# Optimization experiments

Measured on AMD Instinct MI355X. Metric: run time of the kernel, lower is better.

## Reference

```python
import jax, jax.numpy as jnp
import numpy as np

B, L, P, K, D, H = 8192, 224, 6, 5, 128, 4
S = K * K                 # 25 spatial positions in the patch
CENTER = S // 2           # central target pixel index
SCALE_RANGE = 0.2
BN_EPS = 1e-5


def _uniform(k, shape, fan_in):
    s = 1.0 / np.sqrt(fan_in)
    return jax.random.uniform(k, shape, jnp.float32, -s, s)


def setup_inputs() -> dict:
    key = jax.random.key(0)
    ks = jax.random.split(key, 32)
    inp = {}
    inp["x"] = jax.random.normal(ks[0], (B, L, K, K), jnp.float32)
    # attention projections (stored as (in, out), applied as x @ W + b)
    inp["wk_w"] = _uniform(ks[1], (L, D), L); inp["wk_b"] = _uniform(ks[2], (D,), L)
    inp["wv_w"] = _uniform(ks[3], (L, D), L); inp["wv_b"] = _uniform(ks[4], (D,), L)
    inp["wq_w"] = _uniform(ks[5], (L, D), L); inp["wq_b"] = _uniform(ks[6], (D,), L)
    inp["ng_w"] = _uniform(ks[7], (D, 1), D); inp["ng_b"] = _uniform(ks[8], (1,), D)
    # ffn branch: GLU(128->64) -> BN -> GLU(64->P)
    inp["f1_fw"] = _uniform(ks[9], (D, 64), D);  inp["f1_fb"] = _uniform(ks[10], (64,), D)
    inp["f1_gw"] = _uniform(ks[11], (D, 64), D); inp["f1_gb"] = _uniform(ks[12], (64,), D)
    inp["f_bn_g"] = jnp.ones((64,), jnp.float32); inp["f_bn_b"] = jnp.zeros((64,), jnp.float32)
    inp["f2_fw"] = _uniform(ks[13], (64, P), 64); inp["f2_fb"] = _uniform(ks[14], (P,), 64)
    inp["f2_gw"] = _uniform(ks[15], (64, P), 64); inp["f2_gb"] = _uniform(ks[16], (P,), 64)
    # scalar branch: same shapes
    inp["s1_fw"] = _uniform(ks[17], (D, 64), D);  inp["s1_fb"] = _uniform(ks[18], (64,), D)
    inp["s1_gw"] = _uniform(ks[19], (D, 64), D);  inp["s1_gb"] = _uniform(ks[20], (64,), D)
    inp["s_bn_g"] = jnp.ones((64,), jnp.float32); inp["s_bn_b"] = jnp.zeros((64,), jnp.float32)
    inp["s2_fw"] = _uniform(ks[21], (64, P), 64); inp["s2_fb"] = _uniform(ks[22], (P,), 64)
    inp["s2_gw"] = _uniform(ks[23], (64, P), 64); inp["s2_gb"] = _uniform(ks[24], (P,), 64)
    # endmember spectra (P, L), nonnegative as typical for HSI
    inp["endmember"] = jax.random.uniform(ks[25], (P, L), jnp.float32)
    return inp


def _swish(x):
    return x * jax.nn.sigmoid(x)


def _glu(x, fw, fb, gw, gb):
    return (x @ fw + fb) * jax.nn.sigmoid(x @ gw + gb)


def _bn_train(x, g, b):
    # BatchNorm1d training-mode forward: biased batch stats over batch dim
    m = jnp.mean(x, axis=0)
    v = jnp.var(x, axis=0)
    return (x - m) * jax.lax.rsqrt(v + BN_EPS) * g + b


def _forward(x, wk_w, wk_b, wv_w, wv_b, wq_w, wq_b, ng_w, ng_b,
             f1_fw, f1_fb, f1_gw, f1_gb, f_bn_g, f_bn_b, f2_fw, f2_fb, f2_gw, f2_gb,
             s1_fw, s1_fb, s1_gw, s1_gb, s_bn_g, s_bn_b, s2_fw, s2_fb, s2_gw, s2_gb,
             endmember):
    b = x.shape[0]
    xt = x.reshape(b, L, S).transpose(0, 2, 1)        # (B, S, L)
    keys = xt @ wk_w + wk_b                            # (B, S, D)
    vals = xt @ wv_w + wv_b                            # (B, S, D)
    q = xt[:, CENTER] @ wq_w + wq_b                    # (B, D)
    dk, dv = D // H, D // H
    kh = keys.reshape(b, S, H, dk)
    qh = q.reshape(b, H, dk)
    # note: scaling uses full key_dim (np.sqrt(self.key_dim)), not per-head dim
    scores = jnp.einsum('bhd,bshd->bhs', qh, kh) / np.sqrt(D).astype(np.float32)
    mask = jnp.zeros((S,), jnp.float32).at[CENTER].set(-1e6)
    att = jax.nn.softmax(scores + mask, axis=-1)       # (B, H, S)
    vh = vals.reshape(b, S, H, dv)
    surround = jnp.einsum('bhs,bshd->bhd', att, vh).reshape(b, D)
    central = vals[:, CENTER]                          # (B, D)
    nearby = jax.nn.sigmoid((central - surround) @ ng_w + ng_b)  # (B, 1)
    ss = central + nearby * surround                   # (B, D) spatial-spectral feature

    h = _glu(_swish(ss), f1_fw, f1_fb, f1_gw, f1_gb)
    h = _swish(_bn_train(h, f_bn_g, f_bn_b))
    abd = jax.nn.softmax(_glu(h, f2_fw, f2_fb, f2_gw, f2_gb), axis=1)  # (B, P)

    g = _glu(_swish(ss), s1_fw, s1_fb, s1_gw, s1_gb)
    g = _swish(_bn_train(g, s_bn_g, s_bn_b))
    edm_scale = jnp.tanh(_glu(g, s2_fw, s2_fb, s2_gw, s2_gb))          # (B, P)

    scale = 1.0 + SCALE_RANGE * edm_scale[:, :, None]  # (B, P, 1)
    edm = scale * endmember[None]                      # (B, P, L)
    recon = jnp.einsum('bp,bpl->bl', abd, edm)         # (B, L)
    return recon, abd, edm_scale


def reference(x, wk_w, wk_b, wv_w, wv_b, wq_w, wq_b, ng_w, ng_b,
              f1_fw, f1_fb, f1_gw, f1_gb, f_bn_g, f_bn_b, f2_fw, f2_fb, f2_gw, f2_gb,
              s1_fw, s1_fb, s1_gw, s1_gb, s_bn_g, s_bn_b, s2_fw, s2_fb, s2_gw, s2_gb,
              endmember):
    return _forward(x, wk_w, wk_b, wv_w, wv_b, wq_w, wq_b, ng_w, ng_b,
                    f1_fw, f1_fb, f1_gw, f1_gb, f_bn_g, f_bn_b, f2_fw, f2_fb, f2_gw, f2_gb,
                    s1_fw, s1_fb, s1_gw, s1_gb, s_bn_g, s_bn_b, s2_fw, s2_fb, s2_gw, s2_gb,
                    endmember)
```

## Files before the change

### kernel.cpp

```cpp
#include <hip/hip_runtime.h>
#include <hip/hip_bf16.h>

typedef unsigned short ushort;
typedef unsigned int   uint;
typedef __bf16 bfrag_t __attribute__((ext_vector_type(8)));
typedef float  ffrag_t __attribute__((ext_vector_type(4)));

#define NB   8192
#define LL   224
#define SS   25
#define CTR  12
#define DD   128
#define PP   6
#define HID  64
#define GPB  2
#define NKC  7
#define NMT  4
#define NNT  24
#define VST  132
#define WPK_ELEMS (NKC * NNT * 64 * 8)
#define FC1_ELEMS (4 * 16 * 64 * 8)

__device__ __forceinline__ float f_sigmoid(float x) { return 1.0f / (1.0f + __expf(-x)); }
__device__ __forceinline__ ushort f2bf(float f) {
    __hip_bfloat16 h = __float2bfloat16(f);
    ushort u; __builtin_memcpy(&u, &h, 2); return u;
}
__device__ __forceinline__ float bfu2f(ushort u) {
    uint v = ((uint)u) << 16; float f; __builtin_memcpy(&f, &v, 4); return f;
}

__global__ __launch_bounds__(256) void k0_pack(
    const float* __restrict__ wk_w, const float* __restrict__ wv_w,
    const float* __restrict__ wq_w,
    const float* __restrict__ f1_fw, const float* __restrict__ f1_gw,
    const float* __restrict__ s1_fw, const float* __restrict__ s1_gw,
    ushort* __restrict__ wpack, ushort* __restrict__ fc1pack,
    float* __restrict__ stats)
{
    const int blk = blockIdx.x;
    if (blk == 0) stats[threadIdx.x] = 0.f;
    if (blk < NNT) {
        const int nt  = blk;
        const int mat = nt >> 3;
        const float* w = mat == 0 ? wk_w : (mat == 1 ? wv_w : wq_w);
        const int cb = (nt & 7) * 16;
        for (int e = threadIdx.x; e < NKC * 64 * 8; e += 256) {
            int j    = e & 7;
            int lane = (e >> 3) & 63;
            int kc   = e >> 9;
            int k = kc * 32 + ((lane >> 4) << 3) + j;
            int c = cb + (lane & 15);
            wpack[((kc * NNT + nt) * 64 + lane) * 8 + j] = f2bf(w[k * DD + c]);
        }
    } else {
        const int nt = blk - NNT;
        const int m2 = nt >> 2;
        const float* w = m2 == 0 ? f1_fw : (m2 == 1 ? f1_gw : (m2 == 2 ? s1_fw : s1_gw));
        const int cb = (nt & 3) * 16;
        for (int e = threadIdx.x; e < 4 * 64 * 8; e += 256) {
            int j    = e & 7;
            int lane = (e >> 3) & 63;
            int kc   = e >> 9;
            int k = kc * 32 + ((lane >> 4) << 3) + j;
            int c = cb + (lane & 15);
            fc1pack[((kc * 16 + nt) * 64 + lane) * 8 + j] = f2bf(w[k * HID + c]);
        }
    }
}

__global__ __launch_bounds__(512, 4) void kA_front(
    const float* __restrict__ x,
    const ushort* __restrict__ wpack,
    const float* __restrict__ wk_b, const float* __restrict__ wv_b,
    const float* __restrict__ wq_b,
    const float* __restrict__ ng_w, const float* __restrict__ ng_b,
    ushort* __restrict__ swv_ws)
{
    __shared__ ushort alds[NMT * NKC * 64 * 8];
    __shared__ float  qv[GPB * DD];
    __shared__ float  att[8 * 26];
    __shared__ float  red[4];

    const int t    = threadIdx.x;
    const int b0   = blockIdx.x * GPB;
    const int wave = t >> 6;
    const int lane = t & 63;

    const int cC = wave * 16 + (lane & 15);
    const float biask = wk_b[cC];
    const float biasv = wv_b[cC];
    const float biasq = wq_b[cC];
    const float ngw   = ng_w[t & 127];

    const float4* xb4 = (const float4*)(x + (size_t)b0 * (LL * SS));
    float4 xf[6];
#pragma unroll
    for (int k = 0; k < 6; ++k) {
        int q = t + k * 512;
        if (q < 2800) xf[k] = xb4[q];
    }
#pragma unroll
    for (int k = 0; k < 6; ++k) {
        int q = t + k * 512;
        if (q < 2800) {
            int e0 = q * 4;
            int g  = e0 >= 5600;
            int eb0 = e0 - g * 5600;
#pragma unroll
            for (int c = 0; c < 4; ++c) {
                int eb = eb0 + c;
                int l = eb / 25;
                int s = eb - l * 25;
                int r = g * 32 + s;
                int idx = (((r >> 4) * NKC + (l >> 5)) * 64 +
                           ((r & 15) | (((l >> 3) & 3) << 4))) * 8 + (l & 7);
                float fv = c == 0 ? xf[k].x : c == 1 ? xf[k].y : c == 2 ? xf[k].z : xf[k].w;
                alds[idx] = f2bf(fv);
            }
        }
    }
    __syncthreads();

    ffrag_t acck[NMT], accv[NMT], accq[2];
#pragma unroll
    for (int mt = 0; mt < NMT; ++mt) {
        acck[mt] = ffrag_t{0.f, 0.f, 0.f, 0.f};
        accv[mt] = ffrag_t{0.f, 0.f, 0.f, 0.f};
    }
    accq[0] = ffrag_t{0.f, 0.f, 0.f, 0.f};
    accq[1] = ffrag_t{0.f, 0.f, 0.f, 0.f};

    bfrag_t bk = *(const bfrag_t*)(wpack + ((0 * NNT + wave) * 64 + lane) * 8);
    bfrag_t bv = *(const bfrag_t*)(wpack + ((0 * NNT + wave + 8) * 64 + lane) * 8);
    bfrag_t bq = *(const bfrag_t*)(wpack + ((0 * NNT + wave + 16) * 64 + lane) * 8);
#pragma unroll
    for (int kc = 0; kc < NKC; ++kc) {
        bfrag_t nbk, nbv, nbq;
        if (kc + 1 < NKC) {
            nbk = *(const bfrag_t*)(wpack + (((kc + 1) * NNT + wave) * 64 + lane) * 8);
            nbv = *(const bfrag_t*)(wpack + (((kc + 1) * NNT + wave + 8) * 64 + lane) * 8);
            nbq = *(const bfrag_t*)(wpack + (((kc + 1) * NNT + wave + 16) * 64 + lane) * 8);
        }
#pragma unroll
        for (int mt = 0; mt < NMT; ++mt) {
            bfrag_t af = *(const bfrag_t*)(alds + ((mt * NKC + kc) * 64 + lane) * 8);
            acck[mt] = __builtin_amdgcn_mfma_f32_16x16x32_bf16(af, bk, acck[mt], 0, 0, 0);
            accv[mt] = __builtin_amdgcn_mfma_f32_16x16x32_bf16(af, bv, accv[mt], 0, 0, 0);
            if ((mt & 1) == 0)
                accq[mt >> 1] = __builtin_amdgcn_mfma_f32_16x16x32_bf16(af, bq, accq[mt >> 1], 0, 0, 0);
        }
        if (kc + 1 < NKC) { bk = nbk; bv = nbv; bq = nbq; }
    }
    __syncthreads();

    {
#pragma unroll
        for (int mt = 0; mt < NMT; ++mt) {
#pragma unroll
            for (int reg = 0; reg < 4; ++reg) {
                int r = mt * 16 + ((lane >> 4) << 2) + reg;
                int g = r >> 5;
                int s = r & 31;
                if (s < SS) {
                    alds[(g * SS + s) * VST + cC]        = f2bf(acck[mt][reg] + biask);
                    alds[6600 + (g * SS + s) * VST + cC] = f2bf(accv[mt][reg] + biasv);
                }
            }
        }
        if ((lane >> 4) == 3) {
            qv[cC]      = accq[0][0] + biasq;
            qv[DD + cC] = accq[1][0] + biasq;
        }
    }
    __syncthreads();

    if (t < 256) {
        const int r   = t >> 5;
        const int g   = r >> 2;
        const int h   = r & 3;
        const int l32 = t & 31;
        float sc = -1e30f;
        if (l32 < SS) {
            const ushort* kr = alds + (g * SS + l32) * VST + h * 32;
            const float*  qr = qv + g * DD + h * 32;
            float a0 = 0.f, a1 = 0.f, a2 = 0.f, a3 = 0.f;
#pragma unroll
            for (int i = 0; i < 32; i += 4) {
                a0 = fmaf(qr[i + 0], bfu2f(kr[i + 0]), a0);
                a1 = fmaf(qr[i + 1], bfu2f(kr[i + 1]), a1);
                a2 = fmaf(qr[i + 2], bfu2f(kr[i + 2]), a2);
                a3 = fmaf(qr[i + 3], bfu2f(kr[i + 3]), a3);
            }
            sc = ((a0 + a1) + (a2 + a3)) * 0.088388347648318447f;
            if (l32 == CTR) sc -= 1e6f;
        }
        float mx = sc;
#pragma unroll
        for (int m = 16; m > 0; m >>= 1) mx = fmaxf(mx, __shfl_xor(mx, m, 32));
        float e = __expf(sc - mx);
        float sum = e;
#pragma unroll
        for (int m = 16; m > 0; m >>= 1) sum += __shfl_xor(sum, m, 32);
        if (l32 < SS) att[r * 26 + l32] = e / sum;
    }
    __syncthreads();

    if (t < 256) {
        const int g = t >> 7;
        const int d = t & 127;
        const int h = d >> 5;
        const ushort* vrow = alds + 6600 + g * SS * VST + d;
        const float* arow = att + (g * 4 + h) * 26;
        float s0 = 0.f, s1 = 0.f;
#pragma unroll
        for (int s = 0; s < 24; s += 2) {
            s0 = fmaf(arow[s],     bfu2f(vrow[s * VST]),       s0);
            s1 = fmaf(arow[s + 1], bfu2f(vrow[(s + 1) * VST]), s1);
        }
        float sur = fmaf(arow[24], bfu2f(vrow[24 * VST]), s0 + s1);
        float cen = bfu2f(vrow[CTR * VST]);
        float term = (cen - sur) * ngw;
#pragma unroll
        for (int off = 32; off > 0; off >>= 1) term += __shfl_down(term, off);
        if (lane == 0) red[wave] = term;
        __syncthreads();
        float tot = red[g * 2] + red[g * 2 + 1] + ng_b[0];
        float nearby = f_sigmoid(tot);
        float ssv = cen + nearby * sur;
        float sw  = ssv * f_sigmoid(ssv);
        swv_ws[(size_t)(b0 + g) * DD + d] = f2bf(sw);
    } else {
        __syncthreads();
    }
}

__global__ __launch_bounds__(256) void kC_fc1(
    const ushort* __restrict__ swv_ws,
    const ushort* __restrict__ fc1pack,
    const float* __restrict__ f1_fb, const float* __restrict__ f1_gb,
    const float* __restrict__ s1_fb, const float* __restrict__ s1_gb,
    float* __restrict__ h1_ws, float* __restrict__ g1_ws,
    float* __restrict__ stats)
{
    const int t    = threadIdx.x;
    const int wave = t >> 6;
    const int lane = t & 63;
    const int m0   = blockIdx.x * 32;
    const int c16  = wave * 16 + (lane & 15);

    const float fb1 = f1_fb[c16], gb1 = f1_gb[c16];
    const float fb2 = s1_fb[c16], gb2 = s1_gb[c16];

    ffrag_t acc[4][2];
#pragma unroll
    for (int ni = 0; ni < 4; ++ni)
#pragma unroll
        for (int mt = 0; mt < 2; ++mt) acc[ni][mt] = ffrag_t{0.f, 0.f, 0.f, 0.f};

#pragma unroll
    for (int kc = 0; kc < 4; ++kc) {
        bfrag_t bf[4];
#pragma unroll
        for (int ni = 0; ni < 4; ++ni) {
            int nt = wave + 4 * ni;
            bf[ni] = *(const bfrag_t*)(fc1pack + ((kc * 16 + nt) * 64 + lane) * 8);
        }
#pragma unroll
        for (int mt = 0; mt < 2; ++mt) {
            bfrag_t af = *(const bfrag_t*)(swv_ws +
                (size_t)(m0 + mt * 16 + (lane & 15)) * DD + kc * 32 + ((lane >> 4) << 3));
#pragma unroll
            for (int ni = 0; ni < 4; ++ni)
                acc[ni][mt] = __builtin_amdgcn_mfma_f32_16x16x32_bf16(af, bf[ni], acc[ni][mt], 0, 0, 0);
        }
    }

    float hs = 0.f, hq = 0.f, gs = 0.f, gq = 0.f;
#pragma unroll
    for (int mt = 0; mt < 2; ++mt) {
#pragma unroll
        for (int reg = 0; reg < 4; ++reg) {
            int m = m0 + mt * 16 + ((lane >> 4) << 2) + reg;
            float hv = (acc[0][mt][reg] + fb1) * f_sigmoid(acc[1][mt][reg] + gb1);
            float gv = (acc[2][mt][reg] + fb2) * f_sigmoid(acc[3][mt][reg] + gb2);
            h1_ws[(size_t)m * HID + c16] = hv;
            g1_ws[(size_t)m * HID + c16] = gv;
            hs += hv; hq = fmaf(hv, hv, hq);
            gs += gv; gq = fmaf(gv, gv, gq);
        }
    }
    hs += __shfl_xor(hs, 16); hs += __shfl_xor(hs, 32);
    hq += __shfl_xor(hq, 16); hq += __shfl_xor(hq, 32);
    gs += __shfl_xor(gs, 16); gs += __shfl_xor(gs, 32);
    gq += __shfl_xor(gq, 16); gq += __shfl_xor(gq, 32);
    const int cg = lane >> 4;
    float val = cg == 0 ? hs : cg == 1 ? hq : cg == 2 ? gs : gq;
    atomicAdd(&stats[cg * 64 + c16], val);
}

#define K3G 32
__global__ __launch_bounds__(256) void k3_back(
    const float* __restrict__ h1, const float* __restrict__ g1,
    const float* __restrict__ stats,
    const float* __restrict__ f_bng, const float* __restrict__ f_bnb,
    const float* __restrict__ s_bng, const float* __restrict__ s_bnb,
    const float* __restrict__ f2_fw, const float* __restrict__ f2_fb,
    const float* __restrict__ f2_gw, const float* __restrict__ f2_gb,
    const float* __restrict__ s2_fw, const float* __restrict__ s2_fb,
    const float* __restrict__ s2_gw, const float* __restrict__ s2_gb,
    const float* __restrict__ endm,
    float* __restrict__ out_recon, float* __restrict__ out_abd,
    float* __restrict__ out_es)
{
    const int B0 = blockIdx.x * K3G;
    const int t = threadIdx.x;
    __shared__ float bnl[256];
    __shared__ float w2[4][HID * PP];
    __shared__ float b2[4][8];
    __shared__ float endl[PP * LL];
    __shared__ float hh[K3G * 65], gg[K3G * 65];
    __shared__ float logit[K3G * 8], esv[K3G * 8], coef[K3G * 8];

    if (t < 128) {
        int br = t >> 6, j = t & 63;
        float S1 = stats[br * 128 + j];
        float S2 = stats[br * 128 + 64 + j];
        float m   = S1 * (1.0f / NB);
        float var = S2 * (1.0f / NB) - m * m;
        float gam = br ? s_bng[j] : f_bng[j];
        float be  = br ? s_bnb[j] : f_bnb[j];
        float a   = gam * rsqrtf(var + 1e-5f);
        bnl[br * 128 + j]      = a;
        bnl[br * 128 + 64 + j] = be - m * a;
    }
    for (int i = t; i < HID * PP; i += 256) {
        w2[0][i] = f2_fw[i];
        w2[1][i] = f2_gw[i];
        w2[2][i] = s2_fw[i];
        w2[3][i] = s2_gw[i];
    }
    if (t < PP) {
        b2[0][t] = f2_fb[t];
        b2[1][t] = f2_gb[t];
        b2[2][t] = s2_fb[t];
        b2[3][t] = s2_gb[t];
    }
    for (int i = t; i < PP * LL; i += 256) endl[i] = endm[i];
    __syncthreads();

    for (int i = t; i < K3G * HID; i += 256) {
        int ba = i >> 6, j = i & 63;
        float v1 = h1[(size_t)(B0 + ba) * HID + j] * bnl[j] + bnl[64 + j];
        hh[ba * 65 + j] = v1 * f_sigmoid(v1);
        float v2 = g1[(size_t)(B0 + ba) * HID + j] * bnl[128 + j] + bnl[192 + j];
        gg[ba * 65 + j] = v2 * f_sigmoid(v2);
    }
    __syncthreads();

    for (int i = t; i < K3G * 2 * PP; i += 256) {
        int ba = i / (2 * PP);
        int rr = i - ba * (2 * PP);
        int br = rr / PP;
        int p  = rr - br * PP;
        const float* src = (br ? gg : hh) + ba * 65;
        const float* fw  = w2[br * 2];
        const float* gw  = w2[br * 2 + 1];
        float df = b2[br * 2][p], dg = b2[br * 2 + 1][p];
#pragma unroll 8
        for (int j = 0; j < HID; ++j) {
            float v = src[j];
            df = fmaf(v, fw[j * PP + p], df);
            dg = fmaf(v, gw[j * PP + p], dg);
        }
        float glu = df * f_sigmoid(dg);
        if (br == 0) {
            logit[ba * 8 + p] = glu;
        } else {
            float e = tanhf(glu);
            esv[ba * 8 + p] = e;
            out_es[(size_t)(B0 + ba) * PP + p] = e;
        }
    }
    __syncthreads();

    if (t < K3G) {
        float mx = -1e30f;
#pragma unroll
        for (int p = 0; p < PP; ++p) mx = fmaxf(mx, logit[t * 8 + p]);
        float e[PP]; float sum = 0.f;
#pragma unroll
        for (int p = 0; p < PP; ++p) { e[p] = __expf(logit[t * 8 + p] - mx); sum += e[p]; }
        float inv = 1.0f / sum;
#pragma unroll
        for (int p = 0; p < PP; ++p) {
            float a = e[p] * inv;
            out_abd[(size_t)(B0 + t) * PP + p] = a;
            coef[t * 8 + p] = a * (1.0f + 0.2f * esv[t * 8 + p]);
        }
    }
    __syncthreads();

    for (int i = t; i < K3G * LL; i += 256) {
        int ba = i / LL;
        int l  = i - ba * LL;
        float r = 0.f;
#pragma unroll
        for (int p = 0; p < PP; ++p)
            r = fmaf(coef[ba * 8 + p], endl[p * LL + l], r);
        out_recon[(size_t)(B0 + ba) * LL + l] = r;
    }
}

extern "C" void kernel_launch(void* const* d_in, const int* in_sizes, int n_in,
                              void* d_out, int out_size, void* d_ws, size_t ws_size,
                              hipStream_t stream)
{
    const float* x     = (const float*)d_in[0];
    const float* wk_w  = (const float*)d_in[1];
    const float* wk_b  = (const float*)d_in[2];
    const float* wv_w  = (const float*)d_in[3];
    const float* wv_b  = (const float*)d_in[4];
    const float* wq_w  = (const float*)d_in[5];
    const float* wq_b  = (const float*)d_in[6];
    const float* ng_w  = (const float*)d_in[7];
    const float* ng_b  = (const float*)d_in[8];
    const float* f1_fw = (const float*)d_in[9];
    const float* f1_fb = (const float*)d_in[10];
    const float* f1_gw = (const float*)d_in[11];
    const float* f1_gb = (const float*)d_in[12];
    const float* f_bng = (const float*)d_in[13];
    const float* f_bnb = (const float*)d_in[14];
    const float* f2_fw = (const float*)d_in[15];
    const float* f2_fb = (const float*)d_in[16];
    const float* f2_gw = (const float*)d_in[17];
    const float* f2_gb = (const float*)d_in[18];
    const float* s1_fw = (const float*)d_in[19];
    const float* s1_fb = (const float*)d_in[20];
    const float* s1_gw = (const float*)d_in[21];
    const float* s1_gb = (const float*)d_in[22];
    const float* s_bng = (const float*)d_in[23];
    const float* s_bnb = (const float*)d_in[24];
    const float* s2_fw = (const float*)d_in[25];
    const float* s2_fb = (const float*)d_in[26];
    const float* s2_gw = (const float*)d_in[27];
    const float* s2_gb = (const float*)d_in[28];
    const float* endm  = (const float*)d_in[29];

    float* ws = (float*)d_ws;
    float*  h1_ws   = ws;
    float*  g1_ws   = ws + (size_t)NB * HID;
    float*  stats   = ws + 1048576;
    ushort* wpack   = (ushort*)(ws + 1048832);
    ushort* fc1pack = (ushort*)(ws + 1048832 + WPK_ELEMS / 2);
    ushort* swv_ws  = (ushort*)(ws + 1048832 + (WPK_ELEMS + FC1_ELEMS) / 2);

    float* out       = (float*)d_out;
    float* out_recon = out;
    float* out_abd   = out + (size_t)NB * LL;
    float* out_es    = out + (size_t)NB * (LL + PP);

    k0_pack<<<NNT + 16, 256, 0, stream>>>(wk_w, wv_w, wq_w, f1_fw, f1_gw,
                                          s1_fw, s1_gw, wpack, fc1pack, stats);
    kA_front<<<NB / GPB, 512, 0, stream>>>(x, wpack, wk_b, wv_b, wq_b,
                                           ng_w, ng_b, swv_ws);
    kC_fc1<<<NB / 32, 256, 0, stream>>>(swv_ws, fc1pack, f1_fb, f1_gb,
                                        s1_fb, s1_gb, h1_ws, g1_ws, stats);
    k3_back<<<NB / K3G, 256, 0, stream>>>(h1_ws, g1_ws, stats,
                                          f_bng, f_bnb, s_bng, s_bnb,
                                          f2_fw, f2_fb, f2_gw, f2_gb,
                                          s2_fw, s2_fb, s2_gw, s2_gb,
                                          endm, out_recon, out_abd, out_es);
}
```

Baseline: 370.2 us.

## Split attention-score dot products across all threads; simplify index math; shrink k3 group

The attention score stage now uses all 512 threads, with each half-wave computing 16 of the 32 head dims and combining the halves via a cross-lane shuffle, instead of only the first 256 threads doing 32-element dots. The x-to-LDS scatter hoists the divide by 25 out of the inner 4-element loop and replaces it with an incremental wrap. k3_back processes 16 rows per block instead of 32, launching more blocks. These aim to cut per-thread latency in the attention step and improve parallelism in the back kernel, at the cost of an extra shuffle and more blocks in k3.

```diff
diff --git a/kernel.cpp b/kernel.cpp
--- a/kernel.cpp
+++ b/kernel.cpp
@@ -18,6 +18,7 @@
 #define NMT  4
 #define NNT  24
 #define VST  132
+#define VBASE (GPB * SS * VST)
 #define WPK_ELEMS (NKC * NNT * 64 * 8)
 #define FC1_ELEMS (4 * 16 * 64 * 8)
 
@@ -107,11 +108,13 @@
             int e0 = q * 4;
             int g  = e0 >= 5600;
             int eb0 = e0 - g * 5600;
+            int l0 = eb0 / 25;
+            int s0 = eb0 - l0 * 25;
 #pragma unroll
             for (int c = 0; c < 4; ++c) {
-                int eb = eb0 + c;
-                int l = eb / 25;
-                int s = eb - l * 25;
+                int s = s0 + c;
+                int l = l0;
+                if (s >= 25) { s -= 25; ++l; }
                 int r = g * 32 + s;
                 int idx = (((r >> 4) * NKC + (l >> 5)) * 64 +
                            ((r & 15) | (((l >> 3) & 3) << 4))) * 8 + (l & 7);
@@ -163,8 +166,8 @@
                 int g = r >> 5;
                 int s = r & 31;
                 if (s < SS) {
-                    alds[(g * SS + s) * VST + cC]        = f2bf(acck[mt][reg] + biask);
-                    alds[6600 + (g * SS + s) * VST + cC] = f2bf(accv[mt][reg] + biasv);
+                    alds[(g * SS + s) * VST + cC]         = f2bf(acck[mt][reg] + biask);
+                    alds[VBASE + (g * SS + s) * VST + cC] = f2bf(accv[mt][reg] + biasv);
                 }
             }
         }
@@ -175,24 +178,30 @@
     }
     __syncthreads();
 
-    if (t < 256) {
-        const int r   = t >> 5;
-        const int g   = r >> 2;
-        const int h   = r & 3;
-        const int l32 = t & 31;
-        float sc = -1e30f;
+    {
+        const int r    = t >> 6;
+        const int g    = r >> 2;
+        const int h    = r & 3;
+        const int l32  = lane & 31;
+        const int half = lane >> 5;
+        float part = 0.f;
         if (l32 < SS) {
-            const ushort* kr = alds + (g * SS + l32) * VST + h * 32;
-            const float*  qr = qv + g * DD + h * 32;
+            const ushort* kr = alds + (g * SS + l32) * VST + h * 32 + half * 16;
+            const float*  qr = qv + g * DD + h * 32 + half * 16;
             float a0 = 0.f, a1 = 0.f, a2 = 0.f, a3 = 0.f;
 #pragma unroll
-            for (int i = 0; i < 32; i += 4) {
+            for (int i = 0; i < 16; i += 4) {
                 a0 = fmaf(qr[i + 0], bfu2f(kr[i + 0]), a0);
                 a1 = fmaf(qr[i + 1], bfu2f(kr[i + 1]), a1);
                 a2 = fmaf(qr[i + 2], bfu2f(kr[i + 2]), a2);
                 a3 = fmaf(qr[i + 3], bfu2f(kr[i + 3]), a3);
             }
-            sc = ((a0 + a1) + (a2 + a3)) * 0.088388347648318447f;
+            part = (a0 + a1) + (a2 + a3);
+        }
+        part += __shfl_xor(part, 32);
+        float sc = -1e30f;
+        if (l32 < SS) {
+            sc = part * 0.088388347648318447f;
             if (l32 == CTR) sc -= 1e6f;
         }
         float mx = sc;
@@ -202,7 +211,7 @@
         float sum = e;
 #pragma unroll
         for (int m = 16; m > 0; m >>= 1) sum += __shfl_xor(sum, m, 32);
-        if (l32 < SS) att[r * 26 + l32] = e / sum;
+        if (half == 0 && l32 < SS) att[r * 26 + l32] = e / sum;
     }
     __syncthreads();
 
@@ -210,7 +219,7 @@
         const int g = t >> 7;
         const int d = t & 127;
         const int h = d >> 5;
-        const ushort* vrow = alds + 6600 + g * SS * VST + d;
+        const ushort* vrow = alds + VBASE + g * SS * VST + d;
         const float* arow = att + (g * 4 + h) * 26;
         float s0 = 0.f, s1 = 0.f;
 #pragma unroll
@@ -299,7 +308,7 @@
     atomicAdd(&stats[cg * 64 + c16], val);
 }
 
-#define K3G 32
+#define K3G 16
 __global__ __launch_bounds__(256) void k3_back(
     const float* __restrict__ h1, const float* __restrict__ g1,
     const float* __restrict__ stats,
```

After: 365.2 us. About the same (-1.4%).
